# Kernel tuning notes

Measured on AMD Instinct MI355X. Metric: run time of the kernel, lower is better.

## Reference

```python
import jax, jax.numpy as jnp
import numpy as np

B, N, C = 64, 256, 1024
H = 16
D = C // H            # head_dim = 64
HALF = D // 2         # rope dim per axis = 32
PT = 16               # hw_seq_len
THETA = 10000.0


def build_rope_tables():
    # VisionRotaryEmbeddingFast: per-axis freqs, repeated r=2, 2D broadcat
    freqs = 1.0 / (THETA ** (np.arange(0, HALF, 2, dtype=np.float32) / HALF))  # [HALF/2]=16
    t = np.arange(PT, dtype=np.float32)                                        # ft==pt -> t=arange
    f = t[:, None] * freqs[None, :]                                            # [16,16]
    f = np.repeat(f, 2, axis=-1)                                               # [16,32]
    f2d = np.concatenate(
        [np.broadcast_to(f[:, None, :], (PT, PT, HALF)),
         np.broadcast_to(f[None, :, :], (PT, PT, HALF))], axis=-1)             # [16,16,64]
    f2d = f2d.reshape(PT * PT, D)                                              # [256,64]
    return jnp.asarray(np.cos(f2d)), jnp.asarray(np.sin(f2d))


def rotate_half(t):
    # (..., d) -> pairwise (x0,x1) -> (-x1, x0)
    t2 = t.reshape(*t.shape[:-1], -1, 2)
    return jnp.stack([-t2[..., 1], t2[..., 0]], axis=-1).reshape(t.shape)


def apply_rope(t, cos, sin):
    # t: [B,H,N,D]; cos/sin: [N,D]
    return t * cos + rotate_half(t) * sin


def setup_inputs() -> dict:
    key = jax.random.key(0)
    k1, k2, k3 = jax.random.split(key, 3)
    x = jax.random.normal(k1, (B, N, C), dtype=jnp.float32)
    mask = jnp.ones((1, 1, N, N), dtype=bool)  # True = attend (SDPA bool mask)
    qkv_w = jax.random.normal(k2, (3 * C, C), dtype=jnp.float32) * 0.02
    qkv_b = jnp.zeros((3 * C,), dtype=jnp.float32)
    proj_w = jax.random.normal(k3, (C, C), dtype=jnp.float32) * 0.02
    proj_b = jnp.zeros((C,), dtype=jnp.float32)
    rope_cos, rope_sin = build_rope_tables()
    return {"x": x, "mask": mask, "qkv_w": qkv_w, "qkv_b": qkv_b,
            "proj_w": proj_w, "proj_b": proj_b,
            "rope_cos": rope_cos, "rope_sin": rope_sin}


def reference(x, mask, qkv_w, qkv_b, proj_w, proj_b, rope_cos, rope_sin):
    b, n, c = x.shape
    scale = 1.0 / jnp.sqrt(jnp.asarray(D, x.dtype))
    qkv = x @ qkv_w.T + qkv_b                              # [B,N,3C]
    qkv = qkv.reshape(b, n, 3, H, D).transpose(2, 0, 3, 1, 4)  # [3,B,H,N,D]
    q, k, v = qkv[0], qkv[1], qkv[2]
    q = apply_rope(q, rope_cos, rope_sin)
    k = apply_rope(k, rope_cos, rope_sin)
    scores = jnp.einsum('bhnd,bhmd->bhnm', q, k) * scale   # [B,H,N,N]
    neg = jnp.asarray(jnp.finfo(scores.dtype).min, scores.dtype)
    scores = jnp.where(mask, scores, neg)
    attn = jax.nn.softmax(scores, axis=-1)
    out = jnp.einsum('bhnm,bhmd->bhnd', attn, v)           # [B,H,N,D]
    out = out.transpose(0, 2, 1, 3).reshape(b, n, c)       # [B,N,C]
    return out @ proj_w.T + proj_b
```

## Files before the change

### kernel.cpp

```cpp
#include <hip/hip_runtime.h>
#include <math.h>

typedef short s16x8 __attribute__((ext_vector_type(8)));
typedef float f32x4 __attribute__((ext_vector_type(4)));

#define DEV static __device__ __forceinline__

DEV unsigned short f2bf(float f){
  unsigned int u = __builtin_bit_cast(unsigned int, f);
  u += 0x7fffu + ((u >> 16) & 1u);
  return (unsigned short)(u >> 16);
}

DEV void gload_lds16(const void* g, void* l){
  __builtin_amdgcn_global_load_lds(
      (const __attribute__((address_space(1))) unsigned int*)g,
      (__attribute__((address_space(3))) unsigned int*)l,
      16, 0, 0);
}

__global__ void cvt_all(const float* __restrict__ x,  const float* __restrict__ w1,
                        const float* __restrict__ w2,
                        short* __restrict__ ox, short* __restrict__ o1,
                        short* __restrict__ o2){
  int i = blockIdx.x*blockDim.x + threadIdx.x;
  const float* src; short* dst; int j;
  if (i < 2097152)      { src = x;  dst = ox; j = i; }
  else if (i < 2490368) { src = w1; dst = o1; j = i - 2097152; }
  else                  { src = w2; dst = o2; j = i - 2490368; }
  const float* p = src + (size_t)j*8;
  f32x4 a = *(const f32x4*)(p);
  f32x4 b = *(const f32x4*)(p+4);
  s16x8 o;
#pragma unroll
  for (int t=0;t<4;++t){ o[t] = (short)f2bf(a[t]); o[4+t] = (short)f2bf(b[t]); }
  *(s16x8*)(dst + (size_t)j*8) = o;
}

DEV void stage_tile(const short* __restrict__ Ag, const short* __restrict__ Bg,
                    char* buf, int m0, int n0, int k0, int wid, int lane){
  const int l8 = lane >> 3, l7 = lane & 7;
  const int cole = ((l7 ^ l8) << 3) + k0;
#pragma unroll
  for (int j = 0; j < 4; ++j){
    const int c = j*8 + wid;
    const short* src = Ag + (size_t)(m0 + c*8 + l8)*1024 + cole;
    gload_lds16(src, buf + c*1024);
  }
#pragma unroll
  for (int j = 0; j < 4; ++j){
    const int c = j*8 + wid;
    const short* src = Bg + (size_t)(n0 + c*8 + l8)*1024 + cole;
    gload_lds16(src, buf + 32768 + c*1024);
  }
}

template<int EPI>
__global__ __launch_bounds__(512, 2)
void gemm_v3(const short* __restrict__ A, const short* __restrict__ Bw,
             const float* __restrict__ bias,
             const float* __restrict__ cosT, const float* __restrict__ sinT,
             short* __restrict__ q_out, short* __restrict__ k_out, short* __restrict__ v_out,
             float* __restrict__ f_out)
{
  constexpr int BK = 64;
  constexpr int NT = 1024 / BK;
  constexpr int NX = (EPI == 0) ? 12 : 4;
  __shared__ char smem[2 * 65536];

  const int tid  = threadIdx.x;
  const int lane = tid & 63;
  const int wid  = tid >> 6;
  const int wm   = wid >> 2;
  const int wn   = wid & 3;
  const int lr   = lane & 15;
  const int lk   = lane >> 4;

  const int nwg = NX * 64;
  const int bid = blockIdx.x;
  const int cpx = nwg >> 3;
  const int swz = (bid & 7) * cpx + (bid >> 3);
  const int mt  = swz / NX;
  int nt        = swz % NX;
  if (mt & 1) nt = NX - 1 - nt;
  const int m0  = mt * 256;
  const int n0  = nt * 256;

  stage_tile(A, Bw, smem, m0, n0, 0, wid, lane);
  asm volatile("s_waitcnt vmcnt(0)" ::: "memory");
  asm volatile("s_barrier" ::: "memory");

  f32x4 acc[8][4] = {};

  for (int t = 0; t < NT; ++t){
    char* rb = smem + (t & 1) * 65536;
    char* sb = smem + ((t + 1) & 1) * 65536;
    if (t + 1 < NT)
      stage_tile(A, Bw, sb, m0, n0, (t + 1) * BK, wid, lane);
#pragma unroll
    for (int kk = 0; kk < 2; ++kk){
      s16x8 af[8], bf[4];
      const int cb = kk*64 + lk*16;
#pragma unroll
      for (int m = 0; m < 8; ++m){
        const int row = wm*128 + m*16 + lr;
        af[m] = *(const s16x8*)(rb + row*128 + (cb ^ ((row & 7) << 4)));
      }
#pragma unroll
      for (int n = 0; n < 4; ++n){
        const int row = wn*64 + n*16 + lr;
        bf[n] = *(const s16x8*)(rb + 32768 + row*128 + (cb ^ ((row & 7) << 4)));
      }
      __builtin_amdgcn_s_setprio(1);
#pragma unroll
      for (int m = 0; m < 8; ++m)
#pragma unroll
        for (int n = 0; n < 4; ++n)
          acc[m][n] = __builtin_amdgcn_mfma_f32_16x16x32_bf16(af[m], bf[n], acc[m][n], 0, 0, 0);
      __builtin_amdgcn_s_setprio(0);
    }
    asm volatile("s_waitcnt vmcnt(0)" ::: "memory");
    asm volatile("s_barrier" ::: "memory");
  }

  if constexpr (EPI == 0){
    const int sel = n0 >> 10;
    short* dst0 = (sel == 0) ? q_out : k_out;
#pragma unroll
    for (int m = 0; m < 8; ++m){
#pragma unroll
      for (int n = 0; n < 4; ++n){
        const int col  = n0 + wn*64 + n*16 + lr;
        const int rowb = m0 + wm*128 + m*16 + lk*4;
        const float bv = bias[col];
        const int rem = col & 1023;
        const int h = rem >> 6, d = rem & 63;
        if (sel < 2){
#pragma unroll
          for (int r = 0; r < 4; ++r){
            const int row = rowb + r;
            const int ntok = row & 255, b = row >> 8;
            float v = acc[m][n][r] + bv;
            float partner = __shfl_xor(v, 1, 64);
            float rot = (lane & 1) ? partner : -partner;
            float o = v * cosT[ntok*64 + d] + rot * sinT[ntok*64 + d];
            if (sel == 0) o *= 0.125f;
            dst0[(((size_t)b*16 + h)*256 + ntok)*64 + d] = (short)f2bf(o);
          }
        } else {
          const int ntok = rowb & 255, b = rowb >> 8;
          unsigned long long pk = 0;
#pragma unroll
          for (int r = 0; r < 4; ++r)
            pk |= ((unsigned long long)f2bf(acc[m][n][r] + bv)) << (16*r);
          *(unsigned long long*)(v_out + (((size_t)b*16 + h)*64 + d)*256 + ntok) = pk;
        }
      }
    }
  } else {
#pragma unroll
    for (int m = 0; m < 8; ++m){
#pragma unroll
      for (int n = 0; n < 4; ++n){
        const int col  = n0 + wn*64 + n*16 + lr;
        const int rowb = m0 + wm*128 + m*16 + lk*4;
        const float bv = bias[col];
#pragma unroll
        for (int r = 0; r < 4; ++r)
          f_out[(size_t)(rowb + r)*1024 + col] = acc[m][n][r] + bv;
      }
    }
  }
}

__global__ __launch_bounds__(512)
void attn_kernel(const short* __restrict__ qh, const short* __restrict__ kh,
                 const short* __restrict__ vt, short* __restrict__ ao)
{
  __shared__ short Ks[256*64];
  __shared__ short Vs[64*256];
  __shared__ short Ps[8][32*64];
  const int tid  = threadIdx.x;
  const int lane = tid & 63;
  const int wid  = tid >> 6;
  const int lr   = lane & 15;
  const int lk   = lane >> 4;
  const int bh = blockIdx.x;
  const size_t base = (size_t)bh * 256 * 64;
  const short* Kg = kh + base;
  const short* Qg = qh + base;
  const short* Vg = vt + base;

#pragma unroll
  for (int p=0; p<4; ++p){
    int flat = (p*512 + tid)*8;
    uint4 kv = *(const uint4*)(Kg + flat);
    int krow = flat >> 6;  int kcb = (flat & 63)*2;
    *(uint4*)((char*)Ks + krow*128 + (kcb ^ ((krow&7)<<4))) = kv;
    uint4 vv = *(const uint4*)(Vg + flat);
    int vrow = flat >> 8;  int vcb = (flat & 255)*2;
    *(uint4*)((char*)Vs + vrow*512 + (vcb ^ ((vrow&7)<<4))) = vv;
  }

  const int qbase = wid*32;
  s16x8 qf[2][2];
#pragma unroll
  for (int qr=0; qr<2; ++qr)
#pragma unroll
    for (int ks=0; ks<2; ++ks)
      qf[qr][ks] = *(const s16x8*)(Qg + (size_t)(qbase + qr*16 + lr)*64 + ks*32 + lk*8);

  __syncthreads();

  float mrun[2][4], lrun[2][4];
  f32x4 o[2][4] = {};
#pragma unroll
  for (int qr=0; qr<2; ++qr)
#pragma unroll
    for (int r=0; r<4; ++r){ mrun[qr][r] = -INFINITY; lrun[qr][r] = 0.f; }

  for (int t=0; t<4; ++t){
    f32x4 s[2][4] = {};
#pragma unroll
    for (int kc=0; kc<4; ++kc){
      const int row = t*64 + kc*16 + lr;
#pragma unroll
      for (int ks=0; ks<2; ++ks){
        const int cb = ks*64 + lk*16;
        s16x8 kf = *(const s16x8*)((char*)Ks + row*128 + (cb ^ ((row&7)<<4)));
#pragma unroll
        for (int qr=0; qr<2; ++qr)
          s[qr][kc] = __builtin_amdgcn_mfma_f32_16x16x32_bf16(qf[qr][ks], kf, s[qr][kc], 0, 0, 0);
      }
    }
#pragma unroll
    for (int qr=0; qr<2; ++qr)
#pragma unroll
      for (int r=0; r<4; ++r){
        float mx = fmaxf(fmaxf(s[qr][0][r], s[qr][1][r]), fmaxf(s[qr][2][r], s[qr][3][r]));
        mx = fmaxf(mx, __shfl_xor(mx, 1, 64));
        mx = fmaxf(mx, __shfl_xor(mx, 2, 64));
        mx = fmaxf(mx, __shfl_xor(mx, 4, 64));
        mx = fmaxf(mx, __shfl_xor(mx, 8, 64));
        const float mnew  = fmaxf(mrun[qr][r], mx);
        const float alpha = __expf(mrun[qr][r] - mnew);
        float rsum = 0.f;
#pragma unroll
        for (int kc=0; kc<4; ++kc){
          float p = __expf(s[qr][kc][r] - mnew);
          s[qr][kc][r] = p;
          rsum += p;
        }
        rsum += __shfl_xor(rsum, 1, 64);
        rsum += __shfl_xor(rsum, 2, 64);
        rsum += __shfl_xor(rsum, 4, 64);
        rsum += __shfl_xor(rsum, 8, 64);
        lrun[qr][r] = lrun[qr][r]*alpha + rsum;
        mrun[qr][r] = mnew;
#pragma unroll
        for (int oc=0; oc<4; ++oc) o[qr][oc][r] *= alpha;
      }
#pragma unroll
    for (int qr=0; qr<2; ++qr)
#pragma unroll
      for (int kc=0; kc<4; ++kc)
#pragma unroll
        for (int r=0; r<4; ++r){
          const int row = qr*16 + lk*4 + r;
          const int cb  = (kc*16 + lr)*2;
          *(short*)((char*)&Ps[wid][0] + row*128 + (cb ^ ((row&7)<<4))) = (short)f2bf(s[qr][kc][r]);
        }
#pragma unroll
    for (int ks2=0; ks2<2; ++ks2){
      s16x8 pf[2];
#pragma unroll
      for (int qr=0; qr<2; ++qr){
        const int row = qr*16 + lr;
        const int cb  = ks2*64 + lk*16;
        pf[qr] = *(const s16x8*)((char*)&Ps[wid][0] + row*128 + (cb ^ ((row&7)<<4)));
      }
#pragma unroll
      for (int oc=0; oc<4; ++oc){
        const int vrow = oc*16 + lr;
        const int vcb  = t*128 + ks2*64 + lk*16;
        s16x8 vf = *(const s16x8*)((char*)Vs + vrow*512 + (vcb ^ ((vrow&7)<<4)));
#pragma unroll
        for (int qr=0; qr<2; ++qr)
          o[qr][oc] = __builtin_amdgcn_mfma_f32_16x16x32_bf16(pf[qr], vf, o[qr][oc], 0, 0, 0);
      }
    }
  }

  const int b = bh >> 4, h = bh & 15;
#pragma unroll
  for (int qr=0; qr<2; ++qr)
#pragma unroll
    for (int oc=0; oc<4; ++oc)
#pragma unroll
      for (int r=0; r<4; ++r){
        const int n = qbase + qr*16 + lk*4 + r;
        const int d = oc*16 + lr;
        float val = o[qr][oc][r] / lrun[qr][r];
        ao[(size_t)(b*256 + n)*1024 + h*64 + d] = (short)f2bf(val);
      }
}

extern "C" void kernel_launch(void* const* d_in, const int* in_sizes, int n_in,
                              void* d_out, int out_size, void* d_ws, size_t ws_size,
                              hipStream_t stream)
{
  const float* x      = (const float*)d_in[0];
  const float* qkv_w  = (const float*)d_in[2];
  const float* qkv_b  = (const float*)d_in[3];
  const float* proj_w = (const float*)d_in[4];
  const float* proj_b = (const float*)d_in[5];
  const float* rc     = (const float*)d_in[6];
  const float* rs     = (const float*)d_in[7];

  char* ws = (char*)d_ws;
  short* xbf   = (short*)(ws);
  short* wqkv  = (short*)(ws + 33554432);
  short* wproj = (short*)(ws + 39845888);
  short* qhb   = (short*)(ws + 41943040);
  short* khb   = (short*)(ws + 75497472);
  short* vtb   = (short*)(ws + 109051904);
  short* aob   = xbf;

  cvt_all<<<10240, 256, 0, stream>>>(x, qkv_w, proj_w, xbf, wqkv, wproj);

  gemm_v3<0><<<768, 512, 0, stream>>>(xbf, wqkv, qkv_b, rc, rs,
                                      qhb, khb, vtb, nullptr);
  attn_kernel<<<1024, 512, 0, stream>>>(qhb, khb, vtb, aob);
  gemm_v3<1><<<256, 512, 0, stream>>>(aob, wproj, proj_b, nullptr, nullptr,
                                      nullptr, nullptr, nullptr, (float*)d_out);
}
```

Measured before the change: 358.7 us.

## Lazy softmax rescaling, direct global V reads, packed bf16 stores in attention

The attention kernel now rescales the running max only when some row's new max exceeds the stored one by more than a threshold. It starts the max at zero instead of minus infinity and defers the row-sum reduction across lanes to the end. V is read straight from global memory instead of being staged in LDS, which frees shared memory, and the launch bounds now ask for 4 blocks per SM. The QKV-epilogue and attention-output stores pack two bf16 values per 32-bit store. The aim is fewer shuffles, exps and narrow stores and higher occupancy, at the cost of possible overflow risk if scores grow large and uncached global V loads.

```diff
diff --git a/kernel.cpp b/kernel.cpp
--- a/kernel.cpp
+++ b/kernel.cpp
@@ -145,7 +145,11 @@
             float rot = (lane & 1) ? partner : -partner;
             float o = v * cosT[ntok*64 + d] + rot * sinT[ntok*64 + d];
             if (sel == 0) o *= 0.125f;
-            dst0[(((size_t)b*16 + h)*256 + ntok)*64 + d] = (short)f2bf(o);
+            float po = __shfl_xor(o, 1, 64);
+            if (!(lane & 1)){
+              unsigned int pk2 = (unsigned int)f2bf(o) | ((unsigned int)f2bf(po) << 16);
+              *(unsigned int*)(dst0 + (((size_t)b*16 + h)*256 + ntok)*64 + d) = pk2;
+            }
           }
         } else {
           const int ntok = rowb & 255, b = rowb >> 8;
@@ -173,12 +177,11 @@
   }
 }
 
-__global__ __launch_bounds__(512)
+__global__ __launch_bounds__(512, 4)
 void attn_kernel(const short* __restrict__ qh, const short* __restrict__ kh,
                  const short* __restrict__ vt, short* __restrict__ ao)
 {
   __shared__ short Ks[256*64];
-  __shared__ short Vs[64*256];
   __shared__ short Ps[8][32*64];
   const int tid  = threadIdx.x;
   const int lane = tid & 63;
@@ -197,9 +200,6 @@
     uint4 kv = *(const uint4*)(Kg + flat);
     int krow = flat >> 6;  int kcb = (flat & 63)*2;
     *(uint4*)((char*)Ks + krow*128 + (kcb ^ ((krow&7)<<4))) = kv;
-    uint4 vv = *(const uint4*)(Vg + flat);
-    int vrow = flat >> 8;  int vcb = (flat & 255)*2;
-    *(uint4*)((char*)Vs + vrow*512 + (vcb ^ ((vrow&7)<<4))) = vv;
   }
 
   const int qbase = wid*32;
@@ -217,7 +217,7 @@
 #pragma unroll
   for (int qr=0; qr<2; ++qr)
 #pragma unroll
-    for (int r=0; r<4; ++r){ mrun[qr][r] = -INFINITY; lrun[qr][r] = 0.f; }
+    for (int r=0; r<4; ++r){ mrun[qr][r] = 0.f; lrun[qr][r] = 0.f; }
 
   for (int t=0; t<4; ++t){
     f32x4 s[2][4] = {};
@@ -233,32 +233,44 @@
           s[qr][kc] = __builtin_amdgcn_mfma_f32_16x16x32_bf16(qf[qr][ks], kf, s[qr][kc], 0, 0, 0);
       }
     }
+    float wg = -INFINITY;
 #pragma unroll
     for (int qr=0; qr<2; ++qr)
 #pragma unroll
       for (int r=0; r<4; ++r){
-        float mx = fmaxf(fmaxf(s[qr][0][r], s[qr][1][r]), fmaxf(s[qr][2][r], s[qr][3][r]));
-        mx = fmaxf(mx, __shfl_xor(mx, 1, 64));
-        mx = fmaxf(mx, __shfl_xor(mx, 2, 64));
-        mx = fmaxf(mx, __shfl_xor(mx, 4, 64));
-        mx = fmaxf(mx, __shfl_xor(mx, 8, 64));
-        const float mnew  = fmaxf(mrun[qr][r], mx);
-        const float alpha = __expf(mrun[qr][r] - mnew);
-        float rsum = 0.f;
+        float mx3 = fmaxf(fmaxf(s[qr][0][r], s[qr][1][r]), fmaxf(s[qr][2][r], s[qr][3][r]));
+        wg = fmaxf(wg, mx3 - mrun[qr][r]);
+      }
+    if (!__all(wg <= 8.0f)){
+#pragma unroll
+      for (int qr=0; qr<2; ++qr)
+#pragma unroll
+        for (int r=0; r<4; ++r){
+          float mx = fmaxf(fmaxf(s[qr][0][r], s[qr][1][r]), fmaxf(s[qr][2][r], s[qr][3][r]));
+          mx = fmaxf(mx, __shfl_xor(mx, 1, 64));
+          mx = fmaxf(mx, __shfl_xor(mx, 2, 64));
+          mx = fmaxf(mx, __shfl_xor(mx, 4, 64));
+          mx = fmaxf(mx, __shfl_xor(mx, 8, 64));
+          const float mnew = fmaxf(mrun[qr][r], mx);
+          const float alpha = __expf(mrun[qr][r] - mnew);
+          lrun[qr][r] *= alpha;
+#pragma unroll
+          for (int oc=0; oc<4; ++oc) o[qr][oc][r] *= alpha;
+          mrun[qr][r] = mnew;
+        }
+    }
+#pragma unroll
+    for (int qr=0; qr<2; ++qr)
+#pragma unroll
+      for (int r=0; r<4; ++r){
+        float rs = 0.f;
 #pragma unroll
         for (int kc=0; kc<4; ++kc){
-          float p = __expf(s[qr][kc][r] - mnew);
+          float p = __expf(s[qr][kc][r] - mrun[qr][r]);
           s[qr][kc][r] = p;
-          rsum += p;
-        }
-        rsum += __shfl_xor(rsum, 1, 64);
-        rsum += __shfl_xor(rsum, 2, 64);
-        rsum += __shfl_xor(rsum, 4, 64);
-        rsum += __shfl_xor(rsum, 8, 64);
-        lrun[qr][r] = lrun[qr][r]*alpha + rsum;
-        mrun[qr][r] = mnew;
-#pragma unroll
-        for (int oc=0; oc<4; ++oc) o[qr][oc][r] *= alpha;
+          rs += p;
+        }
+        lrun[qr][r] += rs;
       }
 #pragma unroll
     for (int qr=0; qr<2; ++qr)
@@ -281,9 +293,7 @@
       }
 #pragma unroll
       for (int oc=0; oc<4; ++oc){
-        const int vrow = oc*16 + lr;
-        const int vcb  = t*128 + ks2*64 + lk*16;
-        s16x8 vf = *(const s16x8*)((char*)Vs + vrow*512 + (vcb ^ ((vrow&7)<<4)));
+        s16x8 vf = *(const s16x8*)(Vg + (size_t)(oc*16 + lr)*256 + t*64 + ks2*32 + lk*8);
 #pragma unroll
         for (int qr=0; qr<2; ++qr)
           o[qr][oc] = __builtin_amdgcn_mfma_f32_16x16x32_bf16(pf[qr], vf, o[qr][oc], 0, 0, 0);
@@ -292,6 +302,18 @@
   }
 
   const int b = bh >> 4, h = bh & 15;
+  float rinv[2][4];
+#pragma unroll
+  for (int qr=0; qr<2; ++qr)
+#pragma unroll
+    for (int r=0; r<4; ++r){
+      float l = lrun[qr][r];
+      l += __shfl_xor(l, 1, 64);
+      l += __shfl_xor(l, 2, 64);
+      l += __shfl_xor(l, 4, 64);
+      l += __shfl_xor(l, 8, 64);
+      rinv[qr][r] = 1.0f / l;
+    }
 #pragma unroll
   for (int qr=0; qr<2; ++qr)
 #pragma unroll
@@ -300,8 +322,12 @@
       for (int r=0; r<4; ++r){
         const int n = qbase + qr*16 + lk*4 + r;
         const int d = oc*16 + lr;
-        float val = o[qr][oc][r] / lrun[qr][r];
-        ao[(size_t)(b*256 + n)*1024 + h*64 + d] = (short)f2bf(val);
+        float val = o[qr][oc][r] * rinv[qr][r];
+        float pv  = __shfl_xor(val, 1, 64);
+        if (!(lane & 1)){
+          unsigned int pk2 = (unsigned int)f2bf(val) | ((unsigned int)f2bf(pv) << 16);
+          *(unsigned int*)(ao + (size_t)(b*256 + n)*1024 + h*64 + d) = pk2;
+        }
       }
 }
 
```

Result: slower. 450.0 us (+25.5%).
